# Kernel tuning notes

Measured on AMD Instinct MI355X. Metric: run time of the kernel, lower is better.

## Reference

```python
import jax, jax.numpy as jnp
import numpy as np

ALPHA = 2.0  # init kwarg alpha


def _edt(mask):
    """Exact Euclidean distance from each pixel to the nearest False pixel.
    mask: (H, W) bool. Matches scipy.ndimage.distance_transform_edt(mask).
    Separable algorithm: 1D L1 pass along columns, then exact min over columns.
    """
    H, W = mask.shape
    INF = jnp.float32(H + W)
    g0 = jnp.where(mask, INF, 0.0).astype(jnp.float32)  # 0 at background pixels

    def step(carry, row):
        g = jnp.minimum(row, carry + 1.0)
        return g, g

    _, fwd = jax.lax.scan(step, jnp.full((W,), INF, jnp.float32), g0)
    _, bwd = jax.lax.scan(step, jnp.full((W,), INF, jnp.float32), fwd[::-1])
    g = bwd[::-1]  # (H, W): vertical distance to nearest bg in same column

    j = jnp.arange(W, dtype=jnp.float32)
    d2 = (j[:, None] - j[None, :]) ** 2  # (Wj, Wk)
    # dist2[i, j] = min_k g[i, k]^2 + (j - k)^2   -> exact squared EDT
    dist2 = jnp.min(g[:, None, :] ** 2 + d2[None, :, :], axis=-1)  # (H, W)
    return jnp.sqrt(dist2)


def _distance_field(img):
    """img: (N, H, W) float. Replicates LogHausdorffDTLoss.distance_field per slice."""

    def one(ch):
        mask = ch > 0.5
        valid = jnp.logical_and(mask.any(), ~mask.all())
        field = _edt(mask) + _edt(~mask)  # fg_dist + bg_dist
        return jnp.where(valid, field, 0.0)

    # sequential map keeps peak memory to one (H, W, W) intermediate at a time
    return jax.lax.map(one, img)


def setup_inputs() -> dict:
    key = jax.random.key(0)
    k1, k2, k3 = jax.random.split(key, 3)
    B, C, H, W = 8, 4, 256, 256
    preds_S = jax.random.normal(k1, (B, C, H, W), dtype=jnp.float32)
    preds_T = jax.random.normal(k2, (B, C, H, W), dtype=jnp.float32)
    target = jax.random.uniform(k3, (B, 1, H, W), dtype=jnp.float32)
    return {"preds_S": preds_S, "preds_T": preds_T, "target": target}


def reference(preds_S, preds_T, target):
    # shapes already match -> no interpolation; sigmoid=False, softmax=True, C>1
    C = preds_S.shape[1]
    p = jax.nn.softmax(preds_S, axis=1)

    # to_onehot_y=True: target is overwritten by onehot(argmax(teacher)) (detached)
    pT = jax.lax.stop_gradient(preds_T)
    labels = jnp.argmax(pT, axis=1)  # (B, H, W)
    tgt = jax.nn.one_hot(labels, C, axis=1, dtype=p.dtype)  # (B, C, H, W)

    # include_background=False: drop channel 0
    p = p[:, 1:]
    tgt = tgt[:, 1:]
    B, Cc, H, W = p.shape

    pred_dt = _distance_field(jax.lax.stop_gradient(p).reshape(-1, H, W)).reshape(B, Cc, H, W)
    tgt_dt = _distance_field(tgt.reshape(-1, H, W)).reshape(B, Cc, H, W)
    pred_dt = jax.lax.stop_gradient(pred_dt)
    tgt_dt = jax.lax.stop_gradient(tgt_dt)

    err = (p - tgt) ** 2
    dist = pred_dt ** ALPHA + tgt_dt ** ALPHA
    # per-channel means all cover B*H*W elements -> mean of means == global mean
    loss = jnp.mean(err * dist)
    return jnp.log(loss + 1.0)
```

## Files before the change

kernel.cpp:

```cpp
#include <hip/hip_runtime.h>
#include <math.h>

#define HWTOT 65536
#define WD 256
#define HT 256
#define NSL 24

static constexpr size_t OFF_CNT  = 0;
static constexpr size_t OFF_PART = 256;
static constexpr size_t OFF_MASK = 24832;
static constexpr size_t OFF_ERR  = OFF_MASK + (size_t)NSL * HWTOT;
static constexpr size_t OFF_BITS = OFF_ERR + (size_t)NSL * HWTOT * 2;

__global__ __launch_bounds__(256) void k_mask(
    const float* __restrict__ pS, const float* __restrict__ pT,
    unsigned char* __restrict__ mask, _Float16* __restrict__ err)
{
    int blk = blockIdx.x;
    int b   = blk >> 8;
    int hw  = (blk & 255) * 256 + threadIdx.x;

    const float* ps = pS + (size_t)b * 4 * HWTOT + hw;
    float s0 = ps[0], s1 = ps[HWTOT], s2 = ps[2 * HWTOT], s3 = ps[3 * HWTOT];
    float mx = fmaxf(fmaxf(s0, s1), fmaxf(s2, s3));
    float e0 = expf(s0 - mx), e1 = expf(s1 - mx), e2 = expf(s2 - mx), e3 = expf(s3 - mx);
    float inv = 1.0f / (e0 + e1 + e2 + e3);

    const float* pt = pT + (size_t)b * 4 * HWTOT + hw;
    float t0 = pt[0], t1 = pt[HWTOT], t2 = pt[2 * HWTOT], t3 = pt[3 * HWTOT];
    int lab = 0; float bm = t0;
    if (t1 > bm) { bm = t1; lab = 1; }
    if (t2 > bm) { bm = t2; lab = 2; }
    if (t3 > bm) { bm = t3; lab = 3; }

    float pv[3] = { e1 * inv, e2 * inv, e3 * inv };
    #pragma unroll
    for (int cc = 0; cc < 3; ++cc) {
        int sl = b * 3 + cc;
        bool mp = pv[cc] > 0.5f;
        bool mt = (lab == cc + 1);
        mask[(size_t)sl * HWTOT + hw] = (unsigned char)((mp ? 1 : 0) | (mt ? 2 : 0));
        float tcv = mt ? 1.0f : 0.0f;
        float ev = (pv[cc] - tcv) * (pv[cc] - tcv);
        err[(size_t)sl * HWTOT + hw] = (_Float16)ev;
    }
}

__global__ __launch_bounds__(256) void k_pack(
    const unsigned char* __restrict__ mask, unsigned* __restrict__ bits,
    int* __restrict__ cnts)
{
    int s = blockIdx.x;
    int w = threadIdx.x;
    const unsigned char* m = mask + (size_t)s * HWTOT + w;

    int cp = 0, ct = 0;
    #pragma unroll
    for (int k = 0; k < 8; ++k) {
        unsigned vp = 0, vt = 0;
        #pragma unroll
        for (int i = 0; i < 32; ++i) {
            unsigned v = m[(k * 32 + i) * WD];
            vp |= (v & 1u) << i;
            vt |= ((v >> 1) & 1u) << i;
        }
        bits[((size_t)(0 * NSL + s) * 8 + k) * WD + w] = vp;
        bits[((size_t)(1 * NSL + s) * 8 + k) * WD + w] = vt;
        cp += __popc(vp); ct += __popc(vt);
    }

    __shared__ int redc[8];
    #pragma unroll
    for (int i = 1; i < 64; i <<= 1) { cp += __shfl_xor(cp, i); ct += __shfl_xor(ct, i); }
    if ((w & 63) == 0) { redc[w >> 6] = cp; redc[4 + (w >> 6)] = ct; }
    __syncthreads();
    if (w == 0) cnts[s]       = redc[0] + redc[1] + redc[2] + redc[3];
    if (w == 1) cnts[NSL + s] = redc[4] + redc[5] + redc[6] + redc[7];
}

__device__ __forceinline__ int vdist(const unsigned W[8], unsigned inv, int h)
{
    int dd = 512;
    #pragma unroll
    for (int k = 0; k < 8; ++k) {
        unsigned y = W[k] ^ inv;
        unsigned gate;
        if (k * 32 + 31 <= h)      gate = 0u;
        else if (k * 32 > h)       gate = 0xFFFFFFFFu;
        else                       gate = 0xFFFFFFFFu << ((h - k * 32) + 1);
        unsigned z = y & gate;
        int cand = k * 32 + (__ffs(z) - 1) - h;
        dd = (z && dd == 512) ? cand : dd;
    }
    int du = 512;
    #pragma unroll
    for (int k = 7; k >= 0; --k) {
        unsigned y = W[k] ^ inv;
        unsigned gate;
        if (k * 32 >= h)           gate = 0u;
        else if (k * 32 + 32 <= h) gate = 0xFFFFFFFFu;
        else                       gate = (1u << (h - k * 32)) - 1u;
        unsigned z = y & gate;
        int cand = h - (k * 32 + 31 - __clz(z));
        du = (z && du == 512) ? cand : du;
    }
    return min(dd, du);
}

__global__ __launch_bounds__(256) void k_row(
    const _Float16* __restrict__ err, const unsigned* __restrict__ bits,
    const int* __restrict__ cnts, float* __restrict__ partials)
{
    int h  = blockIdx.x;
    int s  = blockIdx.y;
    int jo = threadIdx.x;

    __shared__ float4 g2[768];
    __shared__ float  wred[4];

    const unsigned* bP = bits + (size_t)(0 * NSL + s) * 8 * WD;
    const unsigned* bT = bits + (size_t)(1 * NSL + s) * 8 * WD;
    unsigned WP[8], WT[8];
    #pragma unroll
    for (int k = 0; k < 8; ++k) { WP[k] = bP[k * WD + jo]; WT[k] = bT[k * WD + jo]; }

    int kh = h >> 5, r = h & 31;
    unsigned mywP = 0, mywT = 0;
    #pragma unroll
    for (int k = 0; k < 8; ++k) if (k == kh) { mywP = WP[k]; mywT = WT[k]; }
    bool selP = (mywP >> r) & 1;
    bool selT = (mywT >> r) & 1;

    int gcP = vdist(WP, selP ? 0xFFFFFFFFu : 0u, h);
    int gcT = vdist(WT, selT ? 0xFFFFFFFFu : 0u, h);

    int cp = cnts[s];
    int ct = cnts[NSL + s];
    bool validP = (cp > 0) && (cp < HWTOT);
    bool validT = (ct > 0) && (ct < HWTOT);

    float fP = (float)(gcP * gcP);
    float fT = (float)(gcT * gcT);
    g2[256 + jo] = make_float4(selP ? fP : 0.0f, selP ? 0.0f : fP,
                               selT ? fT : 0.0f, selT ? 0.0f : fT);
    float4 inf4 = make_float4(1e30f, 1e30f, 1e30f, 1e30f);
    g2[jo] = inf4;
    g2[512 + jo] = inf4;

    int gsp = validP ? gcP : 0;
    int gst = validT ? gcT : 0;
    int R = min(max(gsp, gst), 256);
    #pragma unroll
    for (int i = 1; i < 64; i <<= 1) R = max(R, __shfl_xor(R, i));

    float m1 = (float)(gsp * gsp);
    float m2 = (float)(gst * gst);
    __syncthreads();

    for (int dd = 1; dd < R; ++dd) {
        float4 L  = g2[256 + jo - dd];
        float4 Rv = g2[256 + jo + dd];
        float d2 = (float)(dd * dd);
        float c1 = fminf(selP ? L.x : L.y, selP ? Rv.x : Rv.y);
        float c2 = fminf(selT ? L.z : L.w, selT ? Rv.z : Rv.w);
        m1 = fminf(m1, c1 + d2);
        m2 = fminf(m2, c2 + d2);
    }

    size_t rbase = (size_t)s * HWTOT + h * WD + jo;
    float contrib = (float)err[rbase] * (m1 + m2);

    #pragma unroll
    for (int off = 32; off > 0; off >>= 1) contrib += __shfl_down(contrib, off);
    if ((jo & 63) == 0) wred[jo >> 6] = contrib;
    __syncthreads();
    if (jo == 0) partials[s * 256 + h] = wred[0] + wred[1] + wred[2] + wred[3];
}

__global__ __launch_bounds__(256) void k_final(
    const float* __restrict__ partials, float* __restrict__ out)
{
    __shared__ double red[256];
    int t = threadIdx.x;
    double acc = 0.0;
    for (int i = t; i < NSL * 256; i += 256) acc += (double)partials[i];
    red[t] = acc;
    __syncthreads();
    for (int off = 128; off > 0; off >>= 1) {
        if (t < off) red[t] += red[t + off];
        __syncthreads();
    }
    if (t == 0) {
        double loss = red[0] / (double)((size_t)NSL * HWTOT);
        out[0] = (float)log(loss + 1.0);
    }
}

extern "C" void kernel_launch(void* const* d_in, const int* in_sizes, int n_in,
                              void* d_out, int out_size, void* d_ws, size_t ws_size,
                              hipStream_t stream)
{
    const float* pS = (const float*)d_in[0];
    const float* pT = (const float*)d_in[1];
    float* out = (float*)d_out;

    char* ws = (char*)d_ws;
    int*            cnts  = (int*)(ws + OFF_CNT);
    float*          parts = (float*)(ws + OFF_PART);
    unsigned char*  mask  = (unsigned char*)(ws + OFF_MASK);
    _Float16*       err   = (_Float16*)(ws + OFF_ERR);
    unsigned*       bits  = (unsigned*)(ws + OFF_BITS);

    k_mask <<<dim3(2048),     dim3(256), 0, stream>>>(pS, pT, mask, err);
    k_pack <<<dim3(NSL),      dim3(256), 0, stream>>>(mask, bits, cnts);
    k_row  <<<dim3(256, NSL), dim3(256), 0, stream>>>(err, bits, cnts, parts);
    k_final<<<dim3(1),        dim3(256), 0, stream>>>(parts, out);
}
```

Baseline: 113.6 us.

## Split pack kernel across bit-words and fuse final reduction via atomics

The pack kernel now launches one block per slice and 32-row word instead of one block per slice. This raises parallelism from 24 blocks to 192. Validity is now decided from per-word OR/AND reductions instead of popcounts, and k_row reads those reductions. The separate final-reduction kernel is removed: each row block atomically adds its sum into a double accumulator, and the last block to finish computes the log. This saves a launch but adds contention on a global atomic and makes the floating-point summation order nondeterministic.

```diff
diff --git a/kernel.cpp b/kernel.cpp
--- a/kernel.cpp
+++ b/kernel.cpp
@@ -3,12 +3,13 @@
 
 #define HWTOT 65536
 #define WD 256
-#define HT 256
 #define NSL 24
 
-static constexpr size_t OFF_CNT  = 0;
-static constexpr size_t OFF_PART = 256;
-static constexpr size_t OFF_MASK = 24832;
+static constexpr size_t OFF_ACC  = 0;
+static constexpr size_t OFF_DONE = 8;
+static constexpr size_t OFF_OR   = 64;
+static constexpr size_t OFF_AND  = OFF_OR + 2 * NSL * 8 * 4;
+static constexpr size_t OFF_MASK = 4096;
 static constexpr size_t OFF_ERR  = OFF_MASK + (size_t)NSL * HWTOT;
 static constexpr size_t OFF_BITS = OFF_ERR + (size_t)NSL * HWTOT * 2;
 
@@ -48,34 +49,43 @@
 
 __global__ __launch_bounds__(256) void k_pack(
     const unsigned char* __restrict__ mask, unsigned* __restrict__ bits,
-    int* __restrict__ cnts)
+    unsigned* __restrict__ orv, unsigned* __restrict__ andv,
+    double* __restrict__ acc, int* __restrict__ done)
 {
     int s = blockIdx.x;
+    int k = blockIdx.y;
     int w = threadIdx.x;
-    const unsigned char* m = mask + (size_t)s * HWTOT + w;
-
-    int cp = 0, ct = 0;
-    #pragma unroll
-    for (int k = 0; k < 8; ++k) {
-        unsigned vp = 0, vt = 0;
-        #pragma unroll
-        for (int i = 0; i < 32; ++i) {
-            unsigned v = m[(k * 32 + i) * WD];
-            vp |= (v & 1u) << i;
-            vt |= ((v >> 1) & 1u) << i;
-        }
-        bits[((size_t)(0 * NSL + s) * 8 + k) * WD + w] = vp;
-        bits[((size_t)(1 * NSL + s) * 8 + k) * WD + w] = vt;
-        cp += __popc(vp); ct += __popc(vt);
-    }
-
-    __shared__ int redc[8];
-    #pragma unroll
-    for (int i = 1; i < 64; i <<= 1) { cp += __shfl_xor(cp, i); ct += __shfl_xor(ct, i); }
-    if ((w & 63) == 0) { redc[w >> 6] = cp; redc[4 + (w >> 6)] = ct; }
+    const unsigned char* m = mask + (size_t)s * HWTOT + k * 32 * WD + w;
+
+    unsigned vp = 0, vt = 0;
+    #pragma unroll
+    for (int i = 0; i < 32; ++i) {
+        unsigned v = m[i * WD];
+        vp |= (v & 1u) << i;
+        vt |= ((v >> 1) & 1u) << i;
+    }
+    bits[((size_t)(0 * NSL + s) * 8 + k) * WD + w] = vp;
+    bits[((size_t)(1 * NSL + s) * 8 + k) * WD + w] = vt;
+
+    unsigned op = vp, ap = vp, ot = vt, at = vt;
+    #pragma unroll
+    for (int i = 1; i < 64; i <<= 1) {
+        op |= __shfl_xor(op, i); ap &= __shfl_xor(ap, i);
+        ot |= __shfl_xor(ot, i); at &= __shfl_xor(at, i);
+    }
+    __shared__ unsigned ro[4][4];
+    int wv = w >> 6;
+    if ((w & 63) == 0) { ro[wv][0] = op; ro[wv][1] = ap; ro[wv][2] = ot; ro[wv][3] = at; }
     __syncthreads();
-    if (w == 0) cnts[s]       = redc[0] + redc[1] + redc[2] + redc[3];
-    if (w == 1) cnts[NSL + s] = redc[4] + redc[5] + redc[6] + redc[7];
+    if (w == 0) {
+        unsigned OP = ro[0][0] | ro[1][0] | ro[2][0] | ro[3][0];
+        unsigned AP = ro[0][1] & ro[1][1] & ro[2][1] & ro[3][1];
+        unsigned OT = ro[0][2] | ro[1][2] | ro[2][2] | ro[3][2];
+        unsigned AT = ro[0][3] & ro[1][3] & ro[2][3] & ro[3][3];
+        orv [(0 * NSL + s) * 8 + k] = OP;  andv[(0 * NSL + s) * 8 + k] = AP;
+        orv [(1 * NSL + s) * 8 + k] = OT;  andv[(1 * NSL + s) * 8 + k] = AT;
+        if (s == 0 && k == 0) { *acc = 0.0; *done = 0; }
+    }
 }
 
 __device__ __forceinline__ int vdist(const unsigned W[8], unsigned inv, int h)
@@ -109,7 +119,8 @@
 
 __global__ __launch_bounds__(256) void k_row(
     const _Float16* __restrict__ err, const unsigned* __restrict__ bits,
-    const int* __restrict__ cnts, float* __restrict__ partials)
+    const unsigned* __restrict__ orv, const unsigned* __restrict__ andv,
+    double* __restrict__ acc, int* __restrict__ done, float* __restrict__ out)
 {
     int h  = blockIdx.x;
     int s  = blockIdx.y;
@@ -134,10 +145,17 @@
     int gcP = vdist(WP, selP ? 0xFFFFFFFFu : 0u, h);
     int gcT = vdist(WT, selT ? 0xFFFFFFFFu : 0u, h);
 
-    int cp = cnts[s];
-    int ct = cnts[NSL + s];
-    bool validP = (cp > 0) && (cp < HWTOT);
-    bool validT = (ct > 0) && (ct < HWTOT);
+    bool validP, validT;
+    {
+        unsigned OP = 0, AP = 0xFFFFFFFFu, OT = 0, AT = 0xFFFFFFFFu;
+        #pragma unroll
+        for (int k = 0; k < 8; ++k) {
+            OP |= orv[(0 * NSL + s) * 8 + k];  AP &= andv[(0 * NSL + s) * 8 + k];
+            OT |= orv[(1 * NSL + s) * 8 + k];  AT &= andv[(1 * NSL + s) * 8 + k];
+        }
+        validP = (OP != 0u) && (AP != 0xFFFFFFFFu);
+        validT = (OT != 0u) && (AT != 0xFFFFFFFFu);
+    }
 
     float fP = (float)(gcP * gcP);
     float fT = (float)(gcT * gcT);
@@ -174,25 +192,15 @@
     for (int off = 32; off > 0; off >>= 1) contrib += __shfl_down(contrib, off);
     if ((jo & 63) == 0) wred[jo >> 6] = contrib;
     __syncthreads();
-    if (jo == 0) partials[s * 256 + h] = wred[0] + wred[1] + wred[2] + wred[3];
-}
-
-__global__ __launch_bounds__(256) void k_final(
-    const float* __restrict__ partials, float* __restrict__ out)
-{
-    __shared__ double red[256];
-    int t = threadIdx.x;
-    double acc = 0.0;
-    for (int i = t; i < NSL * 256; i += 256) acc += (double)partials[i];
-    red[t] = acc;
-    __syncthreads();
-    for (int off = 128; off > 0; off >>= 1) {
-        if (t < off) red[t] += red[t + off];
-        __syncthreads();
-    }
-    if (t == 0) {
-        double loss = red[0] / (double)((size_t)NSL * HWTOT);
-        out[0] = (float)log(loss + 1.0);
+    if (jo == 0) {
+        float bsum = wred[0] + wred[1] + wred[2] + wred[3];
+        atomicAdd(acc, (double)bsum);
+        __threadfence();
+        int prev = atomicAdd(done, 1);
+        if (prev == NSL * 256 - 1) {
+            double total = atomicAdd(acc, 0.0);
+            out[0] = (float)log(total / (double)((size_t)NSL * HWTOT) + 1.0);
+        }
     }
 }
 
@@ -205,14 +213,15 @@
     float* out = (float*)d_out;
 
     char* ws = (char*)d_ws;
-    int*            cnts  = (int*)(ws + OFF_CNT);
-    float*          parts = (float*)(ws + OFF_PART);
+    double*         acc   = (double*)(ws + OFF_ACC);
+    int*            done  = (int*)(ws + OFF_DONE);
+    unsigned*       orv   = (unsigned*)(ws + OFF_OR);
+    unsigned*       andv  = (unsigned*)(ws + OFF_AND);
     unsigned char*  mask  = (unsigned char*)(ws + OFF_MASK);
     _Float16*       err   = (_Float16*)(ws + OFF_ERR);
     unsigned*       bits  = (unsigned*)(ws + OFF_BITS);
 
     k_mask <<<dim3(2048),     dim3(256), 0, stream>>>(pS, pT, mask, err);
-    k_pack <<<dim3(NSL),      dim3(256), 0, stream>>>(mask, bits, cnts);
-    k_row  <<<dim3(256, NSL), dim3(256), 0, stream>>>(err, bits, cnts, parts);
-    k_final<<<dim3(1),        dim3(256), 0, stream>>>(parts, out);
-}
+    k_pack <<<dim3(NSL, 8),   dim3(256), 0, stream>>>(mask, bits, orv, andv, acc, done);
+    k_row  <<<dim3(256, NSL), dim3(256), 0, stream>>>(err, bits, orv, andv, acc, done, out);
+}
```

New measurement: 224.4 us. 97.5% more time.

## Precompute vertical distances in a separate column-sweep kernel and widen pack grid

Applied to the files above, without the earlier changes.

Adds a k_vgc kernel that computes each column's vertical distance to the nearest differing pixel with forward and backward sweeps per 32-row chunk, storing 16-bit results. k_row then loads these values instead of redoing a bit-scan over 8 words for every pixel. k_pack is split across 8 chunk blocks per slice for more parallelism, and the validity check becomes an OR/AND reduction inside k_vgc instead of popcounts. This costs an extra launch and about 6 MB of extra global traffic for the gc array.

```diff
diff --git a/kernel.cpp b/kernel.cpp
--- a/kernel.cpp
+++ b/kernel.cpp
@@ -3,14 +3,13 @@
 
 #define HWTOT 65536
 #define WD 256
-#define HT 256
 #define NSL 24
 
-static constexpr size_t OFF_CNT  = 0;
 static constexpr size_t OFF_PART = 256;
 static constexpr size_t OFF_MASK = 24832;
 static constexpr size_t OFF_ERR  = OFF_MASK + (size_t)NSL * HWTOT;
 static constexpr size_t OFF_BITS = OFF_ERR + (size_t)NSL * HWTOT * 2;
+static constexpr size_t OFF_GC   = OFF_BITS + (size_t)2 * NSL * 8 * WD * 4;
 
 __global__ __launch_bounds__(256) void k_mask(
     const float* __restrict__ pS, const float* __restrict__ pT,
@@ -47,69 +46,121 @@
 }
 
 __global__ __launch_bounds__(256) void k_pack(
-    const unsigned char* __restrict__ mask, unsigned* __restrict__ bits,
-    int* __restrict__ cnts)
+    const unsigned char* __restrict__ mask, unsigned* __restrict__ bits)
 {
     int s = blockIdx.x;
+    int k = blockIdx.y;
     int w = threadIdx.x;
-    const unsigned char* m = mask + (size_t)s * HWTOT + w;
-
-    int cp = 0, ct = 0;
-    #pragma unroll
-    for (int k = 0; k < 8; ++k) {
-        unsigned vp = 0, vt = 0;
-        #pragma unroll
-        for (int i = 0; i < 32; ++i) {
-            unsigned v = m[(k * 32 + i) * WD];
-            vp |= (v & 1u) << i;
-            vt |= ((v >> 1) & 1u) << i;
+    const unsigned char* m = mask + (size_t)s * HWTOT + k * 32 * WD + w;
+
+    unsigned vp = 0, vt = 0;
+    #pragma unroll
+    for (int i = 0; i < 32; ++i) {
+        unsigned v = m[i * WD];
+        vp |= (v & 1u) << i;
+        vt |= ((v >> 1) & 1u) << i;
+    }
+    bits[((size_t)(0 * NSL + s) * 8 + k) * WD + w] = vp;
+    bits[((size_t)(1 * NSL + s) * 8 + k) * WD + w] = vt;
+}
+
+__device__ __forceinline__ void vgc_field(
+    const unsigned Y[8], bool valid, int kk, int w,
+    unsigned short* __restrict__ gout)
+{
+    unsigned wk = 0;
+    #pragma unroll
+    for (int j = 0; j < 8; ++j) if (j == kk) wk = Y[j];
+
+    int ls = -1000, lc = -1000;
+    #pragma unroll
+    for (int j = 0; j < 8; ++j) {
+        if (j < kk) {
+            unsigned z = Y[j], zc = ~Y[j];
+            ls = z  ? (32 * j + 31 - __clz(z))  : ls;
+            lc = zc ? (32 * j + 31 - __clz(zc)) : lc;
         }
-        bits[((size_t)(0 * NSL + s) * 8 + k) * WD + w] = vp;
-        bits[((size_t)(1 * NSL + s) * 8 + k) * WD + w] = vt;
-        cp += __popc(vp); ct += __popc(vt);
-    }
-
-    __shared__ int redc[8];
-    #pragma unroll
-    for (int i = 1; i < 64; i <<= 1) { cp += __shfl_xor(cp, i); ct += __shfl_xor(ct, i); }
-    if ((w & 63) == 0) { redc[w >> 6] = cp; redc[4 + (w >> 6)] = ct; }
-    __syncthreads();
-    if (w == 0) cnts[s]       = redc[0] + redc[1] + redc[2] + redc[3];
-    if (w == 1) cnts[NSL + s] = redc[4] + redc[5] + redc[6] + redc[7];
-}
-
-__device__ __forceinline__ int vdist(const unsigned W[8], unsigned inv, int h)
-{
-    int dd = 512;
-    #pragma unroll
-    for (int k = 0; k < 8; ++k) {
-        unsigned y = W[k] ^ inv;
-        unsigned gate;
-        if (k * 32 + 31 <= h)      gate = 0u;
-        else if (k * 32 > h)       gate = 0xFFFFFFFFu;
-        else                       gate = 0xFFFFFFFFu << ((h - k * 32) + 1);
-        unsigned z = y & gate;
-        int cand = k * 32 + (__ffs(z) - 1) - h;
-        dd = (z && dd == 512) ? cand : dd;
-    }
-    int du = 512;
-    #pragma unroll
-    for (int k = 7; k >= 0; --k) {
-        unsigned y = W[k] ^ inv;
-        unsigned gate;
-        if (k * 32 >= h)           gate = 0u;
-        else if (k * 32 + 32 <= h) gate = 0xFFFFFFFFu;
-        else                       gate = (1u << (h - k * 32)) - 1u;
-        unsigned z = y & gate;
-        int cand = h - (k * 32 + 31 - __clz(z));
-        du = (z && du == 512) ? cand : du;
-    }
-    return min(dd, du);
+    }
+    unsigned dupk[16];
+    #pragma unroll
+    for (int r = 0; r < 32; ++r) {
+        int h = 32 * kk + r;
+        int b = (wk >> r) & 1;
+        int du = min(h - (b ? lc : ls), 512);
+        if (r & 1) dupk[r >> 1] |= (unsigned)du << 16;
+        else       dupk[r >> 1]  = (unsigned)du;
+        ls = b ? h : ls;
+        lc = b ? lc : h;
+    }
+    int ns = 100000, nc = 100000;
+    #pragma unroll
+    for (int j = 7; j >= 0; --j) {
+        if (j > kk) {
+            unsigned z = Y[j], zc = ~Y[j];
+            ns = z  ? (32 * j + (__ffs(z)  - 1)) : ns;
+            nc = zc ? (32 * j + (__ffs(zc) - 1)) : nc;
+        }
+    }
+    #pragma unroll
+    for (int r = 31; r >= 0; --r) {
+        int h = 32 * kk + r;
+        int b = (wk >> r) & 1;
+        int dd = min((b ? nc : ns) - h, 512);
+        unsigned pk = dupk[r >> 1];
+        int du = (r & 1) ? (int)(pk >> 16) : (int)(pk & 0xffffu);
+        int gcv = min(du, dd);
+        gcv = valid ? gcv : 0;
+        gout[h * WD + w] = (unsigned short)gcv;
+        ns = b ? h : ns;
+        nc = b ? nc : h;
+    }
+}
+
+__global__ __launch_bounds__(256) void k_vgc(
+    const unsigned* __restrict__ bits, unsigned short* __restrict__ gc)
+{
+    int s  = blockIdx.x;
+    int kk = blockIdx.y;
+    int w  = threadIdx.x;
+
+    unsigned YP[8], YT[8];
+    #pragma unroll
+    for (int j = 0; j < 8; ++j) {
+        YP[j] = bits[((size_t)(0 * NSL + s) * 8 + j) * WD + w];
+        YT[j] = bits[((size_t)(1 * NSL + s) * 8 + j) * WD + w];
+    }
+
+    unsigned oP = 0, aP = 0xFFFFFFFFu, oT = 0, aT = 0xFFFFFFFFu;
+    #pragma unroll
+    for (int j = 0; j < 8; ++j) {
+        oP |= YP[j]; aP &= YP[j];
+        oT |= YT[j]; aT &= YT[j];
+    }
+    #pragma unroll
+    for (int i = 1; i < 64; i <<= 1) {
+        oP |= __shfl_xor(oP, i); aP &= __shfl_xor(aP, i);
+        oT |= __shfl_xor(oT, i); aT &= __shfl_xor(aT, i);
+    }
+    __shared__ unsigned rb[4][4];
+    if ((w & 63) == 0) {
+        int wv = w >> 6;
+        rb[wv][0] = oP; rb[wv][1] = aP; rb[wv][2] = oT; rb[wv][3] = aT;
+    }
+    __syncthreads();
+    oP = rb[0][0] | rb[1][0] | rb[2][0] | rb[3][0];
+    aP = rb[0][1] & rb[1][1] & rb[2][1] & rb[3][1];
+    oT = rb[0][2] | rb[1][2] | rb[2][2] | rb[3][2];
+    aT = rb[0][3] & rb[1][3] & rb[2][3] & rb[3][3];
+    bool validP = (oP != 0u) && (aP != 0xFFFFFFFFu);
+    bool validT = (oT != 0u) && (aT != 0xFFFFFFFFu);
+
+    vgc_field(YP, validP, kk, w, gc + (size_t)(0 * NSL + s) * HWTOT);
+    vgc_field(YT, validT, kk, w, gc + (size_t)(1 * NSL + s) * HWTOT);
 }
 
 __global__ __launch_bounds__(256) void k_row(
     const _Float16* __restrict__ err, const unsigned* __restrict__ bits,
-    const int* __restrict__ cnts, float* __restrict__ partials)
+    const unsigned short* __restrict__ gcArr, float* __restrict__ partials)
 {
     int h  = blockIdx.x;
     int s  = blockIdx.y;
@@ -118,26 +169,13 @@
     __shared__ float4 g2[768];
     __shared__ float  wred[4];
 
-    const unsigned* bP = bits + (size_t)(0 * NSL + s) * 8 * WD;
-    const unsigned* bT = bits + (size_t)(1 * NSL + s) * 8 * WD;
-    unsigned WP[8], WT[8];
-    #pragma unroll
-    for (int k = 0; k < 8; ++k) { WP[k] = bP[k * WD + jo]; WT[k] = bT[k * WD + jo]; }
-
-    int kh = h >> 5, r = h & 31;
-    unsigned mywP = 0, mywT = 0;
-    #pragma unroll
-    for (int k = 0; k < 8; ++k) if (k == kh) { mywP = WP[k]; mywT = WT[k]; }
-    bool selP = (mywP >> r) & 1;
-    bool selT = (mywT >> r) & 1;
-
-    int gcP = vdist(WP, selP ? 0xFFFFFFFFu : 0u, h);
-    int gcT = vdist(WT, selT ? 0xFFFFFFFFu : 0u, h);
-
-    int cp = cnts[s];
-    int ct = cnts[NSL + s];
-    bool validP = (cp > 0) && (cp < HWTOT);
-    bool validT = (ct > 0) && (ct < HWTOT);
+    size_t rbase = (size_t)s * HWTOT + h * WD + jo;
+    int gcP = gcArr[rbase];
+    int gcT = gcArr[(size_t)NSL * HWTOT + rbase];
+    unsigned wP = bits[((size_t)(0 * NSL + s) * 8 + (h >> 5)) * WD + jo];
+    unsigned wT = bits[((size_t)(1 * NSL + s) * 8 + (h >> 5)) * WD + jo];
+    bool selP = (wP >> (h & 31)) & 1;
+    bool selT = (wT >> (h & 31)) & 1;
 
     float fP = (float)(gcP * gcP);
     float fT = (float)(gcT * gcT);
@@ -147,14 +185,12 @@
     g2[jo] = inf4;
     g2[512 + jo] = inf4;
 
-    int gsp = validP ? gcP : 0;
-    int gst = validT ? gcT : 0;
-    int R = min(max(gsp, gst), 256);
+    int R = min(max(gcP, gcT), 256);
     #pragma unroll
     for (int i = 1; i < 64; i <<= 1) R = max(R, __shfl_xor(R, i));
 
-    float m1 = (float)(gsp * gsp);
-    float m2 = (float)(gst * gst);
+    float m1 = fP;
+    float m2 = fT;
     __syncthreads();
 
     for (int dd = 1; dd < R; ++dd) {
@@ -167,7 +203,6 @@
         m2 = fminf(m2, c2 + d2);
     }
 
-    size_t rbase = (size_t)s * HWTOT + h * WD + jo;
     float contrib = (float)err[rbase] * (m1 + m2);
 
     #pragma unroll
@@ -205,14 +240,15 @@
     float* out = (float*)d_out;
 
     char* ws = (char*)d_ws;
-    int*            cnts  = (int*)(ws + OFF_CNT);
     float*          parts = (float*)(ws + OFF_PART);
     unsigned char*  mask  = (unsigned char*)(ws + OFF_MASK);
     _Float16*       err   = (_Float16*)(ws + OFF_ERR);
     unsigned*       bits  = (unsigned*)(ws + OFF_BITS);
+    unsigned short* gc    = (unsigned short*)(ws + OFF_GC);
 
     k_mask <<<dim3(2048),     dim3(256), 0, stream>>>(pS, pT, mask, err);
-    k_pack <<<dim3(NSL),      dim3(256), 0, stream>>>(mask, bits, cnts);
-    k_row  <<<dim3(256, NSL), dim3(256), 0, stream>>>(err, bits, cnts, parts);
+    k_pack <<<dim3(NSL, 8),   dim3(256), 0, stream>>>(mask, bits);
+    k_vgc  <<<dim3(NSL, 8),   dim3(256), 0, stream>>>(bits, gc);
+    k_row  <<<dim3(256, NSL), dim3(256), 0, stream>>>(err, bits, gc, parts);
     k_final<<<dim3(1),        dim3(256), 0, stream>>>(parts, out);
 }
```

After: 105.4 us. 1.08x faster.
